# Optimization experiments

Measured on AMD Instinct MI355X. Metric: run time of the kernel, lower is better.

## Reference

```python
import jax, jax.numpy as jnp
import numpy as np
from jax import lax

SKIP = 0.3      # graph_skip_conn
STEPS = 5       # GGNN propagation steps
HEADS = 16
T, B, N, D = 16, 32, 256, 128
NUM_CLASSES = 2
EPS = 1e-8


def setup_inputs() -> dict:
    key = jax.random.key(0)
    ks = jax.random.split(key, 12)
    s = 0.05
    return {
        "inputs": jax.random.normal(ks[0], (T, B, N, D), dtype=jnp.float32),
        "supports": jax.random.uniform(ks[1], (B, N, N), dtype=jnp.float32),
        # multi-head weighted-cosine graph learner weights
        "W_gl": jax.random.normal(ks[2], (HEADS, D), dtype=jnp.float32) * s,
        # GGNN message transform
        "W_a": jax.random.normal(ks[3], (D, D), dtype=jnp.float32) * s,
        "b_a": jnp.zeros((D,), dtype=jnp.float32),
        # GGNN gated propagator (GRU-style) over concat([a, h]) -> D
        "W_r": jax.random.normal(ks[4], (2 * D, D), dtype=jnp.float32) * s,
        "b_r": jnp.zeros((D,), dtype=jnp.float32),
        "W_z": jax.random.normal(ks[5], (2 * D, D), dtype=jnp.float32) * s,
        "b_z": jnp.zeros((D,), dtype=jnp.float32),
        "W_h": jax.random.normal(ks[6], (2 * D, D), dtype=jnp.float32) * s,
        "b_h": jnp.zeros((D,), dtype=jnp.float32),
        # final classifier
        "W_fc": jax.random.normal(ks[7], (N * D, NUM_CLASSES), dtype=jnp.float32) * s,
        "b_fc": jnp.zeros((NUM_CLASSES,), dtype=jnp.float32),
    }


def _cell(x, A, W_gl, W_a, b_a, W_r, b_r, W_z, b_z, W_h, b_h):
    # ---- graph learner: multi-head weighted cosine similarity ----
    # x: (B,N,D); W_gl: (H,D)
    xw = x[None, :, :, :] * W_gl[:, None, None, :]             # (H,B,N,D)
    xw = xw / (jnp.linalg.norm(xw, axis=-1, keepdims=True) + EPS)
    att = jnp.einsum("hbnd,hbmd->hbnm", xw, xw).mean(axis=0)   # (B,N,N)
    att = jax.nn.relu(att)
    att = att / (att.sum(axis=-1, keepdims=True) + EPS)        # row-normalize
    A_new = SKIP * A + (1.0 - SKIP) * att                      # skip connection

    # ---- GGNN propagation over learned adjacency ----
    h = x
    for _ in range(STEPS):
        a = jnp.einsum("bnm,bmd->bnd", A_new, h) @ W_a + b_a   # message
        ah = jnp.concatenate([a, h], axis=-1)                  # (B,N,2D)
        r = jax.nn.sigmoid(ah @ W_r + b_r)
        z = jax.nn.sigmoid(ah @ W_z + b_z)
        h_tilde = jnp.tanh(jnp.concatenate([a, r * h], axis=-1) @ W_h + b_h)
        h = (1.0 - z) * h + z * h_tilde
    return h, A_new


def reference(inputs, supports, W_gl, W_a, b_a, W_r, b_r, W_z, b_z, W_h, b_h, W_fc, b_fc):
    def step(A, x_t):
        h, A_new = _cell(x_t, A, W_gl, W_a, b_a, W_r, b_r, W_z, b_z, W_h, b_h)
        return A_new, h

    A_final, outs = lax.scan(step, supports, inputs)           # outs: (T,B,N,D)
    last = outs[-1]                                            # (B,N,D)
    logits = last.reshape(last.shape[0], -1) @ W_fc + b_fc     # (B,C)
    return logits
```

## Files before the change

kernel.cpp:

```cpp
#include <hip/hip_runtime.h>
#include <math.h>

#define TT 16
#define BB 32
#define NN 256
#define DD 128
#define NSTEPS 5
#define SKIPF 0.3f
#define EPSF 1e-8f


typedef __attribute__((ext_vector_type(8))) short bf16x8;
typedef __attribute__((ext_vector_type(4))) float f32x4;
typedef __attribute__((ext_vector_type(8))) _Float16 half8;
typedef __attribute__((ext_vector_type(2))) _Float16 h2;

__device__ __forceinline__ unsigned short f2bf(float f) {
    union { float f; unsigned u; } v; v.f = f;
    unsigned r = (v.u + 0x7FFF + ((v.u >> 16) & 1)) >> 16;
    return (unsigned short)r;
}
__device__ __forceinline__ float bf2f(unsigned short u) {
    union { unsigned u; float f; } v; v.u = ((unsigned)u) << 16; return v.f;
}
__device__ __forceinline__ unsigned pack2(unsigned short a, unsigned short b) {
    return (unsigned)a | ((unsigned)b << 16);
}
__device__ __forceinline__ unsigned pkrtz(float a, float b) {
    unsigned r;
    asm("v_cvt_pkrtz_f16_f32 %0, %1, %2" : "=v"(r) : "v"(a), "v"(b));
    return r;
}
__device__ __forceinline__ h2 u2h(unsigned u) {
    union { unsigned u; h2 h; } v; v.u = u; return v.h;
}
__device__ __forceinline__ float sigmoidf_(float x) {
    return 1.0f / (1.0f + __expf(-x));
}
__device__ __forceinline__ float tanhf_(float x) {
    return 1.0f - 2.0f / (__expf(2.0f * x) + 1.0f);
}

__global__ __launch_bounds__(256) void k_prep(const float* __restrict__ x,
                                              const unsigned* __restrict__ wsqH,
                                              unsigned short* __restrict__ xh,
                                              unsigned* __restrict__ invnH) {
    int tb = blockIdx.x;
    int tid = threadIdx.x;
    int wave = tid >> 6, lane = tid & 63;
    int m16 = lane & 15, quad = lane >> 4;

    __shared__ unsigned short xsq[256 * 128];

    const float* xb = x + ((size_t)tb << 15);
    unsigned short* xhb = xh + ((size_t)tb << 15);

    #pragma unroll
    for (int it = 0; it < 16; ++it) {
        int flat = (it << 11) + (tid << 3);
        float4 a = *(const float4*)(xb + flat);
        float4 b = *(const float4*)(xb + flat + 4);
        uint4 o;
        o.x = pkrtz(a.x, a.y); o.y = pkrtz(a.z, a.w);
        o.z = pkrtz(b.x, b.y); o.w = pkrtz(b.z, b.w);
        *(uint4*)(xhb + flat) = o;
        uint4 q;
        q.x = pkrtz(a.x * a.x, a.y * a.y); q.y = pkrtz(a.z * a.z, a.w * a.w);
        q.z = pkrtz(b.x * b.x, b.y * b.y); q.w = pkrtz(b.z * b.z, b.w * b.w);
        int row = flat >> 7;
        int byteoff = (flat << 1) ^ ((row & 7) << 4);
        *(uint4*)((char*)xsq + byteoff) = q;
    }
    __syncthreads();

    half8 wf[4];
    #pragma unroll
    for (int ks = 0; ks < 4; ++ks)
        wf[ks] = *(const half8*)((const unsigned short*)wsqH + (m16 << 7) + (ks << 5) + (quad << 3));

    #pragma unroll
    for (int sub = 0; sub < 4; ++sub) {
        int rbase = (wave << 6) + (sub << 4);
        f32x4 acc = (f32x4){0.f, 0.f, 0.f, 0.f};
        #pragma unroll
        for (int ks = 0; ks < 4; ++ks) {
            int row = rbase + m16;
            int byteoff = ((row << 8) + (ks << 6) + (quad << 4)) ^ ((row & 7) << 4);
            half8 af = *(const half8*)((const char*)xsq + byteoff);
            acc = __builtin_amdgcn_mfma_f32_16x16x32_f16(af, wf[ks], acc, 0, 0, 0);
        }
        unsigned out[4];
        #pragma unroll
        for (int r = 0; r < 4; ++r) {
            float inv = 1.0f / (sqrtf(acc[r]) + EPSF);
            out[r] = pkrtz(inv, inv);
        }
        int n = rbase + (quad << 2);
        *(uint4*)(invnH + ((size_t)tb << 12) + (m16 << 8) + n) = *(uint4*)out;
    }
}

__global__ __launch_bounds__(256, 2) void k_gram2(const unsigned short* __restrict__ xhp,
                                                  const unsigned* __restrict__ wsqH,
                                                  const unsigned* __restrict__ invnH,
                                                  unsigned short* __restrict__ attn) {
    int bid = blockIdx.x;
    int tb = bid & 511;
    int rg = bid >> 9;
    int n0 = rg << 6;
    int tid = threadIdx.x;
    int wave = tid >> 6, lane = tid & 63;
    int m16 = lane & 15, quad = lane >> 4;
    int wcol = wave << 6;

    __shared__ unsigned wS[16 * 64];
    __shared__ unsigned ivS[16 * 256];
    __shared__ float rsum[4][64];

    const unsigned short* Xb = xhp + ((size_t)tb << 15);

    {
        uint4 v = *(const uint4*)(wsqH + (tid << 2));
        *(uint4*)(wS + (tid << 2)) = v;
    }
    {
        const unsigned* src = invnH + ((size_t)tb << 12);
        #pragma unroll
        for (int hh = 0; hh < 16; ++hh)
            ivS[(hh << 8) + tid] = src[(hh << 8) + tid];
    }

    half8 Bf[4][4];
    #pragma unroll
    for (int ks = 0; ks < 4; ++ks)
        #pragma unroll
        for (int cb = 0; cb < 4; ++cb)
            Bf[ks][cb] = *(const half8*)(Xb + ((wcol + (cb << 4) + m16) << 7) + (ks << 5) + (quad << 3));

    half8 Af[4][4];
    #pragma unroll
    for (int rb = 0; rb < 4; ++rb)
        #pragma unroll
        for (int ks = 0; ks < 4; ++ks)
            Af[rb][ks] = *(const half8*)(Xb + ((n0 + (rb << 4) + m16) << 7) + (ks << 5) + (quad << 3));

    f32x4 att[4][4];
    #pragma unroll
    for (int rb = 0; rb < 4; ++rb)
        #pragma unroll
        for (int cb = 0; cb < 4; ++cb) att[rb][cb] = (f32x4){0.f, 0.f, 0.f, 0.f};

    __syncthreads();

    union H8 { half8 v; h2 p[4]; };

    #pragma unroll 1
    for (int h = 0; h < 16; ++h) {
        const unsigned* ivh = ivS + (h << 8);
        h2 ivr[4], ivc[4];
        #pragma unroll
        for (int rb = 0; rb < 4; ++rb) ivr[rb] = u2h(ivh[n0 + (rb << 4) + m16]);
        #pragma unroll
        for (int cb = 0; cb < 4; ++cb) ivc[cb] = u2h(ivh[wcol + (cb << 4) + m16]);

        #pragma unroll
        for (int ks = 0; ks < 4; ++ks) {
            uint4 wu = *(const uint4*)(wS + (h << 6) + (ks << 4) + (quad << 2));
            h2 w0 = u2h(wu.x), w1 = u2h(wu.y), w2 = u2h(wu.z), w3 = u2h(wu.w);

            H8 afr[4];
            #pragma unroll
            for (int rb = 0; rb < 4; ++rb) {
                H8 a; a.v = Af[rb][ks];
                h2 s = ivr[rb];
                afr[rb].p[0] = a.p[0] * (w0 * s);
                afr[rb].p[1] = a.p[1] * (w1 * s);
                afr[rb].p[2] = a.p[2] * (w2 * s);
                afr[rb].p[3] = a.p[3] * (w3 * s);
            }
            #pragma unroll
            for (int cb = 0; cb < 4; ++cb) {
                H8 b; b.v = Bf[ks][cb];
                H8 bf;
                bf.p[0] = b.p[0] * ivc[cb];
                bf.p[1] = b.p[1] * ivc[cb];
                bf.p[2] = b.p[2] * ivc[cb];
                bf.p[3] = b.p[3] * ivc[cb];
                #pragma unroll
                for (int rb = 0; rb < 4; ++rb)
                    att[rb][cb] = __builtin_amdgcn_mfma_f32_16x16x32_f16(afr[rb].v, bf.v, att[rb][cb], 0, 0, 0);
            }
        }
    }

    float rs[4][4];
    #pragma unroll
    for (int rb = 0; rb < 4; ++rb)
        #pragma unroll
        for (int r = 0; r < 4; ++r) {
            float s = 0.f;
            #pragma unroll
            for (int cb = 0; cb < 4; ++cb) {
                float v = fmaxf(att[rb][cb][r], 0.0f);
                att[rb][cb][r] = v;
                s += v;
            }
            rs[rb][r] = s;
        }
    #pragma unroll
    for (int m = 1; m < 16; m <<= 1)
        #pragma unroll
        for (int rb = 0; rb < 4; ++rb)
            #pragma unroll
            for (int r = 0; r < 4; ++r)
                rs[rb][r] += __shfl_xor(rs[rb][r], m, 64);
    if (m16 == 0) {
        #pragma unroll
        for (int rb = 0; rb < 4; ++rb)
            #pragma unroll
            for (int r = 0; r < 4; ++r)
                rsum[wave][(rb << 4) + (quad << 2) + r] = rs[rb][r];
    }
    __syncthreads();

    unsigned short* outb = attn + ((size_t)tb << 16);
    #pragma unroll
    for (int rb = 0; rb < 4; ++rb) {
        #pragma unroll
        for (int r = 0; r < 4; ++r) {
            int row = (rb << 4) + (quad << 2) + r;
            float tot = rsum[0][row] + rsum[1][row] + rsum[2][row] + rsum[3][row];
            float inv = (1.0f - SKIPF) / (tot + 16.0f * EPSF);
            #pragma unroll
            for (int cb = 0; cb < 4; ++cb) {
                int col = wcol + (cb << 4) + m16;
                outb[((size_t)(n0 + row) << 8) + col] = f2bf(att[rb][cb][r] * inv);
            }
        }
    }
}

__global__ __launch_bounds__(256) void k_scanlast(const float* __restrict__ supports,
                                                  const unsigned short* __restrict__ AttA,
                                                  unsigned short* __restrict__ Afin) {
    size_t flat = ((size_t)blockIdx.x * 256 + threadIdx.x) * 4;
    float4 s4 = *(const float4*)(supports + flat);
    float a0 = s4.x, a1 = s4.y, a2 = s4.z, a3 = s4.w;
    #pragma unroll
    for (int t = 0; t < TT; ++t) {
        const unsigned short* p = AttA + ((size_t)t << 21) + flat;
        uint2 u = *(const uint2*)p;
        a0 = SKIPF * a0 + bf2f((unsigned short)(u.x & 0xffff));
        a1 = SKIPF * a1 + bf2f((unsigned short)(u.x >> 16));
        a2 = SKIPF * a2 + bf2f((unsigned short)(u.y & 0xffff));
        a3 = SKIPF * a3 + bf2f((unsigned short)(u.y >> 16));
    }
    uint2 o;
    o.x = pack2(f2bf(a0), f2bf(a1));
    o.y = pack2(f2bf(a2), f2bf(a3));
    *(uint2*)(Afin + flat) = o;
}


__global__ __launch_bounds__(256) void k_hTinit(const float* __restrict__ x15,
                                                unsigned short* __restrict__ hT) {
    int bid = blockIdx.x;
    int b = bid >> 5; int r = bid & 31; int d0 = (r >> 3) << 5; int n0 = (r & 7) << 5;
    __shared__ float tl[32][33];
    int tid = threadIdx.x;
    int i = tid >> 5, j = tid & 31;
    #pragma unroll
    for (int s = 0; s < 4; ++s) {
        int nl = (s << 3) + i;
        tl[nl][j] = x15[((size_t)(b * 256 + n0 + nl) << 7) + d0 + j];
    }
    __syncthreads();
    #pragma unroll
    for (int s = 0; s < 4; ++s) {
        int dd = (s << 3) + i;
        hT[((size_t)(b * 128 + d0 + dd) << 8) + n0 + j] = f2bf(tl[j][dd]);
    }
}

__global__ __launch_bounds__(256) void k_wprep(const float* __restrict__ Wa,
                                               const float* __restrict__ Wr,
                                               const float* __restrict__ Wz,
                                               const float* __restrict__ Wh,
                                               const float* __restrict__ Wgl,
                                               unsigned short* __restrict__ WaT,
                                               unsigned short* __restrict__ WrT,
                                               unsigned short* __restrict__ WzT,
                                               unsigned short* __restrict__ WhT,
                                               unsigned* __restrict__ wsqH) {
    int idx = blockIdx.x * 256 + threadIdx.x;
    if (idx < 16384) {
        int dout = idx >> 7, din = idx & 127;
        WaT[idx] = f2bf(Wa[(din << 7) + dout]);
    }
    if (idx < 1024) {
        int h = idx >> 6, j = idx & 63;
        float w0 = Wgl[(h << 7) + (j << 1)];
        float w1 = Wgl[(h << 7) + (j << 1) + 1];
        wsqH[idx] = pkrtz(w0 * w0, w1 * w1);
    }
    {
        int dout = idx >> 8, dk = idx & 255;
        WrT[idx] = f2bf(Wr[(dk << 7) + dout]);
        WzT[idx] = f2bf(Wz[(dk << 7) + dout]);
        WhT[idx] = f2bf(Wh[(dk << 7) + dout]);
    }
}

__global__ __launch_bounds__(256) void k_step(
    const unsigned short* __restrict__ Afin,
    const unsigned short* __restrict__ hT,
    const unsigned short* __restrict__ WaT, const float* __restrict__ ba,
    const unsigned short* __restrict__ WrT, const float* __restrict__ br,
    const unsigned short* __restrict__ WzT, const float* __restrict__ bz,
    const unsigned short* __restrict__ WhT, const float* __restrict__ bh,
    unsigned short* __restrict__ hT_o) {

    int bid = blockIdx.x;
    int b = bid & 31, rg = bid >> 5;
    int n0 = rg << 5;
    int tid = threadIdx.x;
    int wave = tid >> 6, lane = tid & 63;
    int m16 = lane & 15, quad = lane >> 4;
    int wcol = wave << 5;

    __shared__ unsigned short msgS[32 * 136];
    __shared__ unsigned short ahS[32 * 264];

    const unsigned short* hTb = hT + ((size_t)b << 15);

    #pragma unroll
    for (int j = 0; j < 16; ++j) {
        int idx = (j << 8) + tid;
        int d = idx >> 5, row = idx & 31;
        ahS[row * 264 + 128 + d] = hTb[((size_t)d << 8) + n0 + row];
    }

    f32x4 acc[2][2];
    #pragma unroll
    for (int rb = 0; rb < 2; ++rb)
        #pragma unroll
        for (int cb = 0; cb < 2; ++cb) acc[rb][cb] = (f32x4){0.f, 0.f, 0.f, 0.f};

    const unsigned short* Ab = Afin + ((size_t)b << 16) + ((size_t)n0 << 8);
    #pragma unroll 2
    for (int ks = 0; ks < 8; ++ks) {
        bf16x8 af[2], bf[2];
        #pragma unroll
        for (int rb = 0; rb < 2; ++rb)
            af[rb] = *(const bf16x8*)(Ab + (((rb << 4) + m16) << 8) + (ks << 5) + (quad << 3));
        #pragma unroll
        for (int cb = 0; cb < 2; ++cb)
            bf[cb] = *(const bf16x8*)(hTb + ((wcol + (cb << 4) + m16) << 8) + (ks << 5) + (quad << 3));
        #pragma unroll
        for (int rb = 0; rb < 2; ++rb)
            #pragma unroll
            for (int cb = 0; cb < 2; ++cb)
                acc[rb][cb] = __builtin_amdgcn_mfma_f32_16x16x32_bf16(af[rb], bf[cb], acc[rb][cb], 0, 0, 0);
    }
    #pragma unroll
    for (int rb = 0; rb < 2; ++rb)
        #pragma unroll
        for (int cb = 0; cb < 2; ++cb)
            #pragma unroll
            for (int r = 0; r < 4; ++r)
                msgS[((rb << 4) + (quad << 2) + r) * 136 + wcol + (cb << 4) + m16] = f2bf(acc[rb][cb][r]);
    __syncthreads();

    #pragma unroll
    for (int rb = 0; rb < 2; ++rb)
        #pragma unroll
        for (int cb = 0; cb < 2; ++cb) acc[rb][cb] = (f32x4){0.f, 0.f, 0.f, 0.f};
    #pragma unroll
    for (int ks = 0; ks < 4; ++ks) {
        bf16x8 af[2], bf[2];
        #pragma unroll
        for (int rb = 0; rb < 2; ++rb)
            af[rb] = *(const bf16x8*)(msgS + ((rb << 4) + m16) * 136 + (ks << 5) + (quad << 3));
        #pragma unroll
        for (int cb = 0; cb < 2; ++cb)
            bf[cb] = *(const bf16x8*)(WaT + ((wcol + (cb << 4) + m16) << 7) + (ks << 5) + (quad << 3));
        #pragma unroll
        for (int rb = 0; rb < 2; ++rb)
            #pragma unroll
            for (int cb = 0; cb < 2; ++cb)
                acc[rb][cb] = __builtin_amdgcn_mfma_f32_16x16x32_bf16(af[rb], bf[cb], acc[rb][cb], 0, 0, 0);
    }
    {
        float bav[2];
        #pragma unroll
        for (int cb = 0; cb < 2; ++cb) bav[cb] = ba[wcol + (cb << 4) + m16];
        #pragma unroll
        for (int rb = 0; rb < 2; ++rb)
            #pragma unroll
            for (int cb = 0; cb < 2; ++cb)
                #pragma unroll
                for (int r = 0; r < 4; ++r)
                    ahS[((rb << 4) + (quad << 2) + r) * 264 + wcol + (cb << 4) + m16] =
                        f2bf(acc[rb][cb][r] + bav[cb]);
    }
    __syncthreads();

    float hv[2][2][4];
    #pragma unroll
    for (int rb = 0; rb < 2; ++rb)
        #pragma unroll
        for (int cb = 0; cb < 2; ++cb) {
            int col = wcol + (cb << 4) + m16;
            uint2 u = *(const uint2*)(hTb + ((size_t)col << 8) + n0 + (rb << 4) + (quad << 2));
            hv[rb][cb][0] = bf2f((unsigned short)(u.x & 0xffff));
            hv[rb][cb][1] = bf2f((unsigned short)(u.x >> 16));
            hv[rb][cb][2] = bf2f((unsigned short)(u.y & 0xffff));
            hv[rb][cb][3] = bf2f((unsigned short)(u.y >> 16));
        }

    f32x4 racc[2][2], zacc[2][2];
    #pragma unroll
    for (int rb = 0; rb < 2; ++rb)
        #pragma unroll
        for (int cb = 0; cb < 2; ++cb) {
            racc[rb][cb] = (f32x4){0.f, 0.f, 0.f, 0.f};
            zacc[rb][cb] = (f32x4){0.f, 0.f, 0.f, 0.f};
        }
    #pragma unroll 2
    for (int ks = 0; ks < 8; ++ks) {
        bf16x8 af[2], bfr[2], bfz[2];
        #pragma unroll
        for (int rb = 0; rb < 2; ++rb)
            af[rb] = *(const bf16x8*)(ahS + ((rb << 4) + m16) * 264 + (ks << 5) + (quad << 3));
        #pragma unroll
        for (int cb = 0; cb < 2; ++cb) {
            int dout = wcol + (cb << 4) + m16;
            bfr[cb] = *(const bf16x8*)(WrT + (dout << 8) + (ks << 5) + (quad << 3));
            bfz[cb] = *(const bf16x8*)(WzT + (dout << 8) + (ks << 5) + (quad << 3));
        }
        #pragma unroll
        for (int rb = 0; rb < 2; ++rb)
            #pragma unroll
            for (int cb = 0; cb < 2; ++cb) {
                racc[rb][cb] = __builtin_amdgcn_mfma_f32_16x16x32_bf16(af[rb], bfr[cb], racc[rb][cb], 0, 0, 0);
                zacc[rb][cb] = __builtin_amdgcn_mfma_f32_16x16x32_bf16(af[rb], bfz[cb], zacc[rb][cb], 0, 0, 0);
            }
    }
    float zv[2][2][4];
    {
        float brv[2], bzv[2];
        #pragma unroll
        for (int cb = 0; cb < 2; ++cb) {
            brv[cb] = br[wcol + (cb << 4) + m16];
            bzv[cb] = bz[wcol + (cb << 4) + m16];
        }
        #pragma unroll
        for (int rb = 0; rb < 2; ++rb)
            #pragma unroll
            for (int cb = 0; cb < 2; ++cb)
                #pragma unroll
                for (int r = 0; r < 4; ++r) {
                    racc[rb][cb][r] = sigmoidf_(racc[rb][cb][r] + brv[cb]);
                    zv[rb][cb][r]  = sigmoidf_(zacc[rb][cb][r] + bzv[cb]);
                }
    }
    __syncthreads();

    #pragma unroll
    for (int rb = 0; rb < 2; ++rb)
        #pragma unroll
        for (int cb = 0; cb < 2; ++cb)
            #pragma unroll
            for (int r = 0; r < 4; ++r)
                ahS[((rb << 4) + (quad << 2) + r) * 264 + 128 + wcol + (cb << 4) + m16] =
                    f2bf(racc[rb][cb][r] * hv[rb][cb][r]);
    __syncthreads();

    #pragma unroll
    for (int rb = 0; rb < 2; ++rb)
        #pragma unroll
        for (int cb = 0; cb < 2; ++cb) acc[rb][cb] = (f32x4){0.f, 0.f, 0.f, 0.f};
    #pragma unroll 2
    for (int ks = 0; ks < 8; ++ks) {
        bf16x8 af[2], bf[2];
        #pragma unroll
        for (int rb = 0; rb < 2; ++rb)
            af[rb] = *(const bf16x8*)(ahS + ((rb << 4) + m16) * 264 + (ks << 5) + (quad << 3));
        #pragma unroll
        for (int cb = 0; cb < 2; ++cb)
            bf[cb] = *(const bf16x8*)(WhT + ((wcol + (cb << 4) + m16) << 8) + (ks << 5) + (quad << 3));
        #pragma unroll
        for (int rb = 0; rb < 2; ++rb)
            #pragma unroll
            for (int cb = 0; cb < 2; ++cb)
                acc[rb][cb] = __builtin_amdgcn_mfma_f32_16x16x32_bf16(af[rb], bf[cb], acc[rb][cb], 0, 0, 0);
    }

    {
        float bhv[2];
        #pragma unroll
        for (int cb = 0; cb < 2; ++cb) bhv[cb] = bh[wcol + (cb << 4) + m16];
        #pragma unroll
        for (int rb = 0; rb < 2; ++rb)
            #pragma unroll
            for (int cb = 0; cb < 2; ++cb) {
                int col = wcol + (cb << 4) + m16;
                unsigned short pk[4];
                #pragma unroll
                for (int r = 0; r < 4; ++r) {
                    float ht = tanhf_(acc[rb][cb][r] + bhv[cb]);
                    float hn = hv[rb][cb][r] + zv[rb][cb][r] * (ht - hv[rb][cb][r]);
                    pk[r] = f2bf(hn);
                }
                uint2 p;
                p.x = pack2(pk[0], pk[1]); p.y = pack2(pk[2], pk[3]);
                *(uint2*)(hT_o + ((size_t)(b * 128 + col) << 8) + n0 + (rb << 4) + (quad << 2)) = p;
            }
    }
}

__global__ __launch_bounds__(256) void k_fc(const unsigned short* __restrict__ hT,
                                            const float* __restrict__ Wfc,
                                            const float* __restrict__ bfc,
                                            float* __restrict__ out) {
    int bid = blockIdx.x;
    int b = bid >> 4, part = bid & 15;
    int tid = threadIdx.x;
    const unsigned short* hp = hT + ((size_t)b << 15);
    int i = part * 2048 + tid * 8;
    int d = i >> 8, n = i & 255;
    uint4 hu = *(const uint4*)(hp + i);
    unsigned short hs[8];
    hs[0] = hu.x & 0xffff; hs[1] = hu.x >> 16;
    hs[2] = hu.y & 0xffff; hs[3] = hu.y >> 16;
    hs[4] = hu.z & 0xffff; hs[5] = hu.z >> 16;
    hs[6] = hu.w & 0xffff; hs[7] = hu.w >> 16;
    float a0 = 0.f, a1 = 0.f;
    #pragma unroll
    for (int k = 0; k < 8; ++k) {
        float v = bf2f(hs[k]);
        const float2 w = *(const float2*)(Wfc + ((size_t)(n + k) * 128 + d) * 2);
        a0 = fmaf(v, w.x, a0);
        a1 = fmaf(v, w.y, a1);
    }
    int wave = tid >> 6, lane = tid & 63;
    #pragma unroll
    for (int off = 32; off; off >>= 1) {
        a0 += __shfl_down(a0, off, 64);
        a1 += __shfl_down(a1, off, 64);
    }
    __shared__ float r0[4], r1[4];
    if (lane == 0) { r0[wave] = a0; r1[wave] = a1; }
    __syncthreads();
    if (tid == 0) {
        float s0 = r0[0] + r0[1] + r0[2] + r0[3];
        float s1 = r1[0] + r1[1] + r1[2] + r1[3];
        if (part == 0) { s0 += bfc[0]; s1 += bfc[1]; }
        atomicAdd(&out[b * 2 + 0], s0);
        atomicAdd(&out[b * 2 + 1], s1);
    }
}

extern "C" void kernel_launch(void* const* d_in, const int* in_sizes, int n_in,
                              void* d_out, int out_size, void* d_ws, size_t ws_size,
                              hipStream_t stream) {
    const float* x_all    = (const float*)d_in[0];
    const float* supports = (const float*)d_in[1];
    const float* Wgl = (const float*)d_in[2];
    const float* Wa  = (const float*)d_in[3];
    const float* ba  = (const float*)d_in[4];
    const float* Wr  = (const float*)d_in[5];
    const float* br  = (const float*)d_in[6];
    const float* Wz  = (const float*)d_in[7];
    const float* bz  = (const float*)d_in[8];
    const float* Wh  = (const float*)d_in[9];
    const float* bh  = (const float*)d_in[10];
    const float* Wfc = (const float*)d_in[11];
    const float* bfc = (const float*)d_in[12];
    float* out = (float*)d_out;

    char* p = (char*)d_ws;
    auto alloc = [&](size_t bytes) { char* r = p; p += (bytes + 255) & ~(size_t)255; return r; };

    unsigned short* AttA = (unsigned short*)alloc((size_t)TT * BB * NN * NN * 2);
    unsigned short* xh   = (unsigned short*)alloc((size_t)TT * BB * NN * DD * 2);
    unsigned* invnH      = (unsigned*)alloc((size_t)TT * BB * 16 * NN * 4);
    unsigned short* Afin = (unsigned short*)alloc((size_t)BB * NN * NN * 2);
    unsigned short* hT0  = (unsigned short*)alloc((size_t)BB * DD * NN * 2);
    unsigned short* hT1  = (unsigned short*)alloc((size_t)BB * DD * NN * 2);
    unsigned short* WaT  = (unsigned short*)alloc(128 * 128 * 2);
    unsigned short* WrT  = (unsigned short*)alloc(256 * 128 * 2);
    unsigned short* WzT  = (unsigned short*)alloc(256 * 128 * 2);
    unsigned short* WhT  = (unsigned short*)alloc(256 * 128 * 2);
    unsigned* wsqH       = (unsigned*)alloc(16 * 64 * 4);

    k_wprep<<<128, 256, 0, stream>>>(Wa, Wr, Wz, Wh, Wgl, WaT, WrT, WzT, WhT, wsqH);
    k_prep<<<TT * BB, 256, 0, stream>>>(x_all, wsqH, xh, invnH);

    k_gram2<<<4 * TT * BB, 256, 0, stream>>>(xh, wsqH, invnH, AttA);
    k_scanlast<<<2048, 256, 0, stream>>>(supports, AttA, Afin);

    const float* x15 = x_all + (size_t)15 * BB * NN * DD;
    k_hTinit<<<BB * 32, 256, 0, stream>>>(x15, hT0);

    const unsigned short* hT_in = hT0;
    for (int s = 0; s < NSTEPS; ++s) {
        unsigned short* hTo = (s & 1) ? hT0 : hT1;
        k_step<<<8 * BB, 256, 0, stream>>>(Afin, hT_in,
                                           WaT, ba, WrT, br, WzT, bz, WhT, bh,
                                           hTo);
        hT_in = hTo;
    }
    hipMemsetAsync(d_out, 0, (size_t)out_size * sizeof(float), stream);
    k_fc<<<BB * 16, 256, 0, stream>>>(hT1, Wfc, bfc, out);
}
```

Measured before the change: 363.6 us.

## Fuse GGNN steps, init transpose and FC into one persistent kernel with per-batch barriers

Replaces the hT init kernel, five per-step launches and the FC kernel with a single launch of 256 blocks. The eight blocks of each batch synchronise through global atomic counters between propagation steps. The FC reduction is done directly from registers in the last step, so the final h is never written back. This removes seven kernel launches and their gaps, at the cost of spin-wait barriers that rely on all 256 blocks being co-resident.

```diff
diff --git a/kernel.cpp b/kernel.cpp
--- a/kernel.cpp
+++ b/kernel.cpp
@@ -39,6 +39,18 @@
 }
 __device__ __forceinline__ float tanhf_(float x) {
     return 1.0f - 2.0f / (__expf(2.0f * x) + 1.0f);
+}
+
+__device__ __forceinline__ void bbar(int* c) {
+    __syncthreads();
+    __threadfence();
+    if (threadIdx.x == 0) {
+        __hip_atomic_fetch_add(c, 1, __ATOMIC_RELEASE, __HIP_MEMORY_SCOPE_AGENT);
+        while (__hip_atomic_load(c, __ATOMIC_ACQUIRE, __HIP_MEMORY_SCOPE_AGENT) < 8)
+            __builtin_amdgcn_s_sleep(2);
+    }
+    __syncthreads();
+    (void)__hip_atomic_load(c, __ATOMIC_ACQUIRE, __HIP_MEMORY_SCOPE_AGENT);
 }
 
 __global__ __launch_bounds__(256) void k_prep(const float* __restrict__ x,
@@ -261,27 +273,6 @@
     *(uint2*)(Afin + flat) = o;
 }
 
-
-__global__ __launch_bounds__(256) void k_hTinit(const float* __restrict__ x15,
-                                                unsigned short* __restrict__ hT) {
-    int bid = blockIdx.x;
-    int b = bid >> 5; int r = bid & 31; int d0 = (r >> 3) << 5; int n0 = (r & 7) << 5;
-    __shared__ float tl[32][33];
-    int tid = threadIdx.x;
-    int i = tid >> 5, j = tid & 31;
-    #pragma unroll
-    for (int s = 0; s < 4; ++s) {
-        int nl = (s << 3) + i;
-        tl[nl][j] = x15[((size_t)(b * 256 + n0 + nl) << 7) + d0 + j];
-    }
-    __syncthreads();
-    #pragma unroll
-    for (int s = 0; s < 4; ++s) {
-        int dd = (s << 3) + i;
-        hT[((size_t)(b * 128 + d0 + dd) << 8) + n0 + j] = f2bf(tl[j][dd]);
-    }
-}
-
 __global__ __launch_bounds__(256) void k_wprep(const float* __restrict__ Wa,
                                                const float* __restrict__ Wr,
                                                const float* __restrict__ Wz,
@@ -311,14 +302,16 @@
     }
 }
 
-__global__ __launch_bounds__(256) void k_step(
+__global__ __launch_bounds__(256) void k_gru(
+    const float* __restrict__ x15,
     const unsigned short* __restrict__ Afin,
-    const unsigned short* __restrict__ hT,
     const unsigned short* __restrict__ WaT, const float* __restrict__ ba,
     const unsigned short* __restrict__ WrT, const float* __restrict__ br,
     const unsigned short* __restrict__ WzT, const float* __restrict__ bz,
     const unsigned short* __restrict__ WhT, const float* __restrict__ bh,
-    unsigned short* __restrict__ hT_o) {
+    const float* __restrict__ Wfc, const float* __restrict__ bfc,
+    unsigned short* __restrict__ hTa, unsigned short* __restrict__ hTbuf,
+    int* __restrict__ cnt, float* __restrict__ out) {
 
     int bid = blockIdx.x;
     int b = bid & 31, rg = bid >> 5;
@@ -330,232 +323,247 @@
 
     __shared__ unsigned short msgS[32 * 136];
     __shared__ unsigned short ahS[32 * 264];
-
-    const unsigned short* hTb = hT + ((size_t)b << 15);
-
-    #pragma unroll
-    for (int j = 0; j < 16; ++j) {
-        int idx = (j << 8) + tid;
-        int d = idx >> 5, row = idx & 31;
-        ahS[row * 264 + 128 + d] = hTb[((size_t)d << 8) + n0 + row];
-    }
-
-    f32x4 acc[2][2];
-    #pragma unroll
-    for (int rb = 0; rb < 2; ++rb)
-        #pragma unroll
-        for (int cb = 0; cb < 2; ++cb) acc[rb][cb] = (f32x4){0.f, 0.f, 0.f, 0.f};
-
+    __shared__ float rf0[4], rf1[4];
+
+    int* cbp = cnt + b * 5;
+
+    {
+        float* tl = (float*)ahS;
+        int i = tid >> 5, j = tid & 31;
+        for (int dt = 0; dt < 4; ++dt) {
+            int d0 = dt << 5;
+            #pragma unroll
+            for (int s4 = 0; s4 < 4; ++s4) {
+                int nl = (s4 << 3) + i;
+                tl[nl * 33 + j] = x15[((size_t)(b * 256 + n0 + nl) << 7) + d0 + j];
+            }
+            __syncthreads();
+            #pragma unroll
+            for (int s4 = 0; s4 < 4; ++s4) {
+                int dd = (s4 << 3) + i;
+                hTa[((size_t)(b * 128 + d0 + dd) << 8) + n0 + j] = f2bf(tl[j * 33 + dd]);
+            }
+            __syncthreads();
+        }
+    }
+    bbar(cbp + 0);
+
+    float fca = 0.f, fcb = 0.f;
     const unsigned short* Ab = Afin + ((size_t)b << 16) + ((size_t)n0 << 8);
-    #pragma unroll 2
-    for (int ks = 0; ks < 8; ++ks) {
-        bf16x8 af[2], bf[2];
+
+    for (int s = 0; s < NSTEPS; ++s) {
+        const unsigned short* hTin = (s & 1) ? hTbuf : hTa;
+        unsigned short* hTo = (s & 1) ? hTa : hTbuf;
+        const unsigned short* hTb = hTin + ((size_t)b << 15);
+
+        #pragma unroll
+        for (int j = 0; j < 16; ++j) {
+            int idx = (j << 8) + tid;
+            int d = idx >> 5, row = idx & 31;
+            ahS[row * 264 + 128 + d] = hTb[((size_t)d << 8) + n0 + row];
+        }
+
+        f32x4 acc[2][2];
         #pragma unroll
         for (int rb = 0; rb < 2; ++rb)
-            af[rb] = *(const bf16x8*)(Ab + (((rb << 4) + m16) << 8) + (ks << 5) + (quad << 3));
-        #pragma unroll
-        for (int cb = 0; cb < 2; ++cb)
-            bf[cb] = *(const bf16x8*)(hTb + ((wcol + (cb << 4) + m16) << 8) + (ks << 5) + (quad << 3));
+            #pragma unroll
+            for (int cb = 0; cb < 2; ++cb) acc[rb][cb] = (f32x4){0.f, 0.f, 0.f, 0.f};
+
+        #pragma unroll 2
+        for (int ks = 0; ks < 8; ++ks) {
+            bf16x8 af[2], bf[2];
+            #pragma unroll
+            for (int rb = 0; rb < 2; ++rb)
+                af[rb] = *(const bf16x8*)(Ab + (((rb << 4) + m16) << 8) + (ks << 5) + (quad << 3));
+            #pragma unroll
+            for (int cb = 0; cb < 2; ++cb)
+                bf[cb] = *(const bf16x8*)(hTb + ((wcol + (cb << 4) + m16) << 8) + (ks << 5) + (quad << 3));
+            #pragma unroll
+            for (int rb = 0; rb < 2; ++rb)
+                #pragma unroll
+                for (int cb = 0; cb < 2; ++cb)
+                    acc[rb][cb] = __builtin_amdgcn_mfma_f32_16x16x32_bf16(af[rb], bf[cb], acc[rb][cb], 0, 0, 0);
+        }
         #pragma unroll
         for (int rb = 0; rb < 2; ++rb)
             #pragma unroll
             for (int cb = 0; cb < 2; ++cb)
-                acc[rb][cb] = __builtin_amdgcn_mfma_f32_16x16x32_bf16(af[rb], bf[cb], acc[rb][cb], 0, 0, 0);
-    }
-    #pragma unroll
-    for (int rb = 0; rb < 2; ++rb)
-        #pragma unroll
-        for (int cb = 0; cb < 2; ++cb)
-            #pragma unroll
-            for (int r = 0; r < 4; ++r)
-                msgS[((rb << 4) + (quad << 2) + r) * 136 + wcol + (cb << 4) + m16] = f2bf(acc[rb][cb][r]);
-    __syncthreads();
-
-    #pragma unroll
-    for (int rb = 0; rb < 2; ++rb)
-        #pragma unroll
-        for (int cb = 0; cb < 2; ++cb) acc[rb][cb] = (f32x4){0.f, 0.f, 0.f, 0.f};
-    #pragma unroll
-    for (int ks = 0; ks < 4; ++ks) {
-        bf16x8 af[2], bf[2];
+                #pragma unroll
+                for (int r = 0; r < 4; ++r)
+                    msgS[((rb << 4) + (quad << 2) + r) * 136 + wcol + (cb << 4) + m16] = f2bf(acc[rb][cb][r]);
+        __syncthreads();
+
         #pragma unroll
         for (int rb = 0; rb < 2; ++rb)
-            af[rb] = *(const bf16x8*)(msgS + ((rb << 4) + m16) * 136 + (ks << 5) + (quad << 3));
-        #pragma unroll
-        for (int cb = 0; cb < 2; ++cb)
-            bf[cb] = *(const bf16x8*)(WaT + ((wcol + (cb << 4) + m16) << 7) + (ks << 5) + (quad << 3));
-        #pragma unroll
-        for (int rb = 0; rb < 2; ++rb)
+            #pragma unroll
+            for (int cb = 0; cb < 2; ++cb) acc[rb][cb] = (f32x4){0.f, 0.f, 0.f, 0.f};
+        #pragma unroll
+        for (int ks = 0; ks < 4; ++ks) {
+            bf16x8 af[2], bf[2];
+            #pragma unroll
+            for (int rb = 0; rb < 2; ++rb)
+                af[rb] = *(const bf16x8*)(msgS + ((rb << 4) + m16) * 136 + (ks << 5) + (quad << 3));
             #pragma unroll
             for (int cb = 0; cb < 2; ++cb)
-                acc[rb][cb] = __builtin_amdgcn_mfma_f32_16x16x32_bf16(af[rb], bf[cb], acc[rb][cb], 0, 0, 0);
-    }
-    {
-        float bav[2];
-        #pragma unroll
-        for (int cb = 0; cb < 2; ++cb) bav[cb] = ba[wcol + (cb << 4) + m16];
-        #pragma unroll
-        for (int rb = 0; rb < 2; ++rb)
-            #pragma unroll
-            for (int cb = 0; cb < 2; ++cb)
-                #pragma unroll
-                for (int r = 0; r < 4; ++r)
-                    ahS[((rb << 4) + (quad << 2) + r) * 264 + wcol + (cb << 4) + m16] =
-                        f2bf(acc[rb][cb][r] + bav[cb]);
-    }
-    __syncthreads();
-
-    float hv[2][2][4];
-    #pragma unroll
-    for (int rb = 0; rb < 2; ++rb)
-        #pragma unroll
-        for (int cb = 0; cb < 2; ++cb) {
-            int col = wcol + (cb << 4) + m16;
-            uint2 u = *(const uint2*)(hTb + ((size_t)col << 8) + n0 + (rb << 4) + (quad << 2));
-            hv[rb][cb][0] = bf2f((unsigned short)(u.x & 0xffff));
-            hv[rb][cb][1] = bf2f((unsigned short)(u.x >> 16));
-            hv[rb][cb][2] = bf2f((unsigned short)(u.y & 0xffff));
-            hv[rb][cb][3] = bf2f((unsigned short)(u.y >> 16));
-        }
-
-    f32x4 racc[2][2], zacc[2][2];
-    #pragma unroll
-    for (int rb = 0; rb < 2; ++rb)
-        #pragma unroll
-        for (int cb = 0; cb < 2; ++cb) {
-            racc[rb][cb] = (f32x4){0.f, 0.f, 0.f, 0.f};
-            zacc[rb][cb] = (f32x4){0.f, 0.f, 0.f, 0.f};
-        }
-    #pragma unroll 2
-    for (int ks = 0; ks < 8; ++ks) {
-        bf16x8 af[2], bfr[2], bfz[2];
-        #pragma unroll
-        for (int rb = 0; rb < 2; ++rb)
-            af[rb] = *(const bf16x8*)(ahS + ((rb << 4) + m16) * 264 + (ks << 5) + (quad << 3));
-        #pragma unroll
-        for (int cb = 0; cb < 2; ++cb) {
-            int dout = wcol + (cb << 4) + m16;
-            bfr[cb] = *(const bf16x8*)(WrT + (dout << 8) + (ks << 5) + (quad << 3));
-            bfz[cb] = *(const bf16x8*)(WzT + (dout << 8) + (ks << 5) + (quad << 3));
-        }
-        #pragma unroll
-        for (int rb = 0; rb < 2; ++rb)
-            #pragma unroll
-            for (int cb = 0; cb < 2; ++cb) {
-                racc[rb][cb] = __builtin_amdgcn_mfma_f32_16x16x32_bf16(af[rb], bfr[cb], racc[rb][cb], 0, 0, 0);
-                zacc[rb][cb] = __builtin_amdgcn_mfma_f32_16x16x32_bf16(af[rb], bfz[cb], zacc[rb][cb], 0, 0, 0);
-            }
-    }
-    float zv[2][2][4];
-    {
-        float brv[2], bzv[2];
-        #pragma unroll
-        for (int cb = 0; cb < 2; ++cb) {
-            brv[cb] = br[wcol + (cb << 4) + m16];
-            bzv[cb] = bz[wcol + (cb << 4) + m16];
-        }
-        #pragma unroll
-        for (int rb = 0; rb < 2; ++rb)
-            #pragma unroll
-            for (int cb = 0; cb < 2; ++cb)
-                #pragma unroll
-                for (int r = 0; r < 4; ++r) {
-                    racc[rb][cb][r] = sigmoidf_(racc[rb][cb][r] + brv[cb]);
-                    zv[rb][cb][r]  = sigmoidf_(zacc[rb][cb][r] + bzv[cb]);
-                }
-    }
-    __syncthreads();
-
-    #pragma unroll
-    for (int rb = 0; rb < 2; ++rb)
-        #pragma unroll
-        for (int cb = 0; cb < 2; ++cb)
-            #pragma unroll
-            for (int r = 0; r < 4; ++r)
-                ahS[((rb << 4) + (quad << 2) + r) * 264 + 128 + wcol + (cb << 4) + m16] =
-                    f2bf(racc[rb][cb][r] * hv[rb][cb][r]);
-    __syncthreads();
-
-    #pragma unroll
-    for (int rb = 0; rb < 2; ++rb)
-        #pragma unroll
-        for (int cb = 0; cb < 2; ++cb) acc[rb][cb] = (f32x4){0.f, 0.f, 0.f, 0.f};
-    #pragma unroll 2
-    for (int ks = 0; ks < 8; ++ks) {
-        bf16x8 af[2], bf[2];
-        #pragma unroll
-        for (int rb = 0; rb < 2; ++rb)
-            af[rb] = *(const bf16x8*)(ahS + ((rb << 4) + m16) * 264 + (ks << 5) + (quad << 3));
-        #pragma unroll
-        for (int cb = 0; cb < 2; ++cb)
-            bf[cb] = *(const bf16x8*)(WhT + ((wcol + (cb << 4) + m16) << 8) + (ks << 5) + (quad << 3));
-        #pragma unroll
-        for (int rb = 0; rb < 2; ++rb)
-            #pragma unroll
-            for (int cb = 0; cb < 2; ++cb)
-                acc[rb][cb] = __builtin_amdgcn_mfma_f32_16x16x32_bf16(af[rb], bf[cb], acc[rb][cb], 0, 0, 0);
-    }
-
-    {
-        float bhv[2];
-        #pragma unroll
-        for (int cb = 0; cb < 2; ++cb) bhv[cb] = bh[wcol + (cb << 4) + m16];
+                bf[cb] = *(const bf16x8*)(WaT + ((wcol + (cb << 4) + m16) << 7) + (ks << 5) + (quad << 3));
+            #pragma unroll
+            for (int rb = 0; rb < 2; ++rb)
+                #pragma unroll
+                for (int cb = 0; cb < 2; ++cb)
+                    acc[rb][cb] = __builtin_amdgcn_mfma_f32_16x16x32_bf16(af[rb], bf[cb], acc[rb][cb], 0, 0, 0);
+        }
+        {
+            float bav[2];
+            #pragma unroll
+            for (int cb = 0; cb < 2; ++cb) bav[cb] = ba[wcol + (cb << 4) + m16];
+            #pragma unroll
+            for (int rb = 0; rb < 2; ++rb)
+                #pragma unroll
+                for (int cb = 0; cb < 2; ++cb)
+                    #pragma unroll
+                    for (int r = 0; r < 4; ++r)
+                        ahS[((rb << 4) + (quad << 2) + r) * 264 + wcol + (cb << 4) + m16] =
+                            f2bf(acc[rb][cb][r] + bav[cb]);
+        }
+        __syncthreads();
+
+        float hv[2][2][4];
         #pragma unroll
         for (int rb = 0; rb < 2; ++rb)
             #pragma unroll
             for (int cb = 0; cb < 2; ++cb) {
                 int col = wcol + (cb << 4) + m16;
-                unsigned short pk[4];
-                #pragma unroll
-                for (int r = 0; r < 4; ++r) {
-                    float ht = tanhf_(acc[rb][cb][r] + bhv[cb]);
-                    float hn = hv[rb][cb][r] + zv[rb][cb][r] * (ht - hv[rb][cb][r]);
-                    pk[r] = f2bf(hn);
+                uint2 u = *(const uint2*)(hTb + ((size_t)col << 8) + n0 + (rb << 4) + (quad << 2));
+                hv[rb][cb][0] = bf2f((unsigned short)(u.x & 0xffff));
+                hv[rb][cb][1] = bf2f((unsigned short)(u.x >> 16));
+                hv[rb][cb][2] = bf2f((unsigned short)(u.y & 0xffff));
+                hv[rb][cb][3] = bf2f((unsigned short)(u.y >> 16));
+            }
+
+        f32x4 racc[2][2], zacc[2][2];
+        #pragma unroll
+        for (int rb = 0; rb < 2; ++rb)
+            #pragma unroll
+            for (int cb = 0; cb < 2; ++cb) {
+                racc[rb][cb] = (f32x4){0.f, 0.f, 0.f, 0.f};
+                zacc[rb][cb] = (f32x4){0.f, 0.f, 0.f, 0.f};
+            }
+        #pragma unroll 2
+        for (int ks = 0; ks < 8; ++ks) {
+            bf16x8 af[2], bfr[2], bfz[2];
+            #pragma unroll
+            for (int rb = 0; rb < 2; ++rb)
+                af[rb] = *(const bf16x8*)(ahS + ((rb << 4) + m16) * 264 + (ks << 5) + (quad << 3));
+            #pragma unroll
+            for (int cb = 0; cb < 2; ++cb) {
+                int dout = wcol + (cb << 4) + m16;
+                bfr[cb] = *(const bf16x8*)(WrT + (dout << 8) + (ks << 5) + (quad << 3));
+                bfz[cb] = *(const bf16x8*)(WzT + (dout << 8) + (ks << 5) + (quad << 3));
+            }
+            #pragma unroll
+            for (int rb = 0; rb < 2; ++rb)
+                #pragma unroll
+                for (int cb = 0; cb < 2; ++cb) {
+                    racc[rb][cb] = __builtin_amdgcn_mfma_f32_16x16x32_bf16(af[rb], bfr[cb], racc[rb][cb], 0, 0, 0);
+                    zacc[rb][cb] = __builtin_amdgcn_mfma_f32_16x16x32_bf16(af[rb], bfz[cb], zacc[rb][cb], 0, 0, 0);
                 }
-                uint2 p;
-                p.x = pack2(pk[0], pk[1]); p.y = pack2(pk[2], pk[3]);
-                *(uint2*)(hT_o + ((size_t)(b * 128 + col) << 8) + n0 + (rb << 4) + (quad << 2)) = p;
-            }
-    }
-}
-
-__global__ __launch_bounds__(256) void k_fc(const unsigned short* __restrict__ hT,
-                                            const float* __restrict__ Wfc,
-                                            const float* __restrict__ bfc,
-                                            float* __restrict__ out) {
-    int bid = blockIdx.x;
-    int b = bid >> 4, part = bid & 15;
-    int tid = threadIdx.x;
-    const unsigned short* hp = hT + ((size_t)b << 15);
-    int i = part * 2048 + tid * 8;
-    int d = i >> 8, n = i & 255;
-    uint4 hu = *(const uint4*)(hp + i);
-    unsigned short hs[8];
-    hs[0] = hu.x & 0xffff; hs[1] = hu.x >> 16;
-    hs[2] = hu.y & 0xffff; hs[3] = hu.y >> 16;
-    hs[4] = hu.z & 0xffff; hs[5] = hu.z >> 16;
-    hs[6] = hu.w & 0xffff; hs[7] = hu.w >> 16;
-    float a0 = 0.f, a1 = 0.f;
-    #pragma unroll
-    for (int k = 0; k < 8; ++k) {
-        float v = bf2f(hs[k]);
-        const float2 w = *(const float2*)(Wfc + ((size_t)(n + k) * 128 + d) * 2);
-        a0 = fmaf(v, w.x, a0);
-        a1 = fmaf(v, w.y, a1);
-    }
-    int wave = tid >> 6, lane = tid & 63;
+        }
+        float zv[2][2][4];
+        {
+            float brv[2], bzv[2];
+            #pragma unroll
+            for (int cb = 0; cb < 2; ++cb) {
+                brv[cb] = br[wcol + (cb << 4) + m16];
+                bzv[cb] = bz[wcol + (cb << 4) + m16];
+            }
+            #pragma unroll
+            for (int rb = 0; rb < 2; ++rb)
+                #pragma unroll
+                for (int cb = 0; cb < 2; ++cb)
+                    #pragma unroll
+                    for (int r = 0; r < 4; ++r) {
+                        racc[rb][cb][r] = sigmoidf_(racc[rb][cb][r] + brv[cb]);
+                        zv[rb][cb][r]  = sigmoidf_(zacc[rb][cb][r] + bzv[cb]);
+                    }
+        }
+        __syncthreads();
+
+        #pragma unroll
+        for (int rb = 0; rb < 2; ++rb)
+            #pragma unroll
+            for (int cb = 0; cb < 2; ++cb)
+                #pragma unroll
+                for (int r = 0; r < 4; ++r)
+                    ahS[((rb << 4) + (quad << 2) + r) * 264 + 128 + wcol + (cb << 4) + m16] =
+                        f2bf(racc[rb][cb][r] * hv[rb][cb][r]);
+        __syncthreads();
+
+        #pragma unroll
+        for (int rb = 0; rb < 2; ++rb)
+            #pragma unroll
+            for (int cb = 0; cb < 2; ++cb) acc[rb][cb] = (f32x4){0.f, 0.f, 0.f, 0.f};
+        #pragma unroll 2
+        for (int ks = 0; ks < 8; ++ks) {
+            bf16x8 af[2], bf[2];
+            #pragma unroll
+            for (int rb = 0; rb < 2; ++rb)
+                af[rb] = *(const bf16x8*)(ahS + ((rb << 4) + m16) * 264 + (ks << 5) + (quad << 3));
+            #pragma unroll
+            for (int cb = 0; cb < 2; ++cb)
+                bf[cb] = *(const bf16x8*)(WhT + ((wcol + (cb << 4) + m16) << 8) + (ks << 5) + (quad << 3));
+            #pragma unroll
+            for (int rb = 0; rb < 2; ++rb)
+                #pragma unroll
+                for (int cb = 0; cb < 2; ++cb)
+                    acc[rb][cb] = __builtin_amdgcn_mfma_f32_16x16x32_bf16(af[rb], bf[cb], acc[rb][cb], 0, 0, 0);
+        }
+
+        {
+            float bhv[2];
+            #pragma unroll
+            for (int cb = 0; cb < 2; ++cb) bhv[cb] = bh[wcol + (cb << 4) + m16];
+            #pragma unroll
+            for (int rb = 0; rb < 2; ++rb)
+                #pragma unroll
+                for (int cb = 0; cb < 2; ++cb) {
+                    int col = wcol + (cb << 4) + m16;
+                    unsigned short pk[4];
+                    #pragma unroll
+                    for (int r = 0; r < 4; ++r) {
+                        float ht = tanhf_(acc[rb][cb][r] + bhv[cb]);
+                        float hn = hv[rb][cb][r] + zv[rb][cb][r] * (ht - hv[rb][cb][r]);
+                        pk[r] = f2bf(hn);
+                    }
+                    if (s < NSTEPS - 1) {
+                        uint2 p;
+                        p.x = pack2(pk[0], pk[1]); p.y = pack2(pk[2], pk[3]);
+                        *(uint2*)(hTo + ((size_t)(b * 128 + col) << 8) + n0 + (rb << 4) + (quad << 2)) = p;
+                    } else {
+                        #pragma unroll
+                        for (int r = 0; r < 4; ++r) {
+                            int nn = n0 + (rb << 4) + (quad << 2) + r;
+                            float hval = bf2f(pk[r]);
+                            const float2 w = *(const float2*)(Wfc + (size_t)(nn * 128 + col) * 2);
+                            fca = fmaf(hval, w.x, fca);
+                            fcb = fmaf(hval, w.y, fcb);
+                        }
+                    }
+                }
+        }
+        if (s < NSTEPS - 1) bbar(cbp + 1 + s);
+    }
+
     #pragma unroll
     for (int off = 32; off; off >>= 1) {
-        a0 += __shfl_down(a0, off, 64);
-        a1 += __shfl_down(a1, off, 64);
-    }
-    __shared__ float r0[4], r1[4];
-    if (lane == 0) { r0[wave] = a0; r1[wave] = a1; }
+        fca += __shfl_down(fca, off, 64);
+        fcb += __shfl_down(fcb, off, 64);
+    }
+    if (lane == 0) { rf0[wave] = fca; rf1[wave] = fcb; }
     __syncthreads();
     if (tid == 0) {
-        float s0 = r0[0] + r0[1] + r0[2] + r0[3];
-        float s1 = r1[0] + r1[1] + r1[2] + r1[3];
-        if (part == 0) { s0 += bfc[0]; s1 += bfc[1]; }
+        float s0 = rf0[0] + rf0[1] + rf0[2] + rf0[3];
+        float s1 = rf1[0] + rf1[1] + rf1[2] + rf1[3];
+        if (rg == 0) { s0 += bfc[0]; s1 += bfc[1]; }
         atomicAdd(&out[b * 2 + 0], s0);
         atomicAdd(&out[b * 2 + 1], s1);
     }
@@ -593,6 +601,10 @@
     unsigned short* WzT  = (unsigned short*)alloc(256 * 128 * 2);
     unsigned short* WhT  = (unsigned short*)alloc(256 * 128 * 2);
     unsigned* wsqH       = (unsigned*)alloc(16 * 64 * 4);
+    int* cntB            = (int*)alloc(32 * 5 * 4);
+
+    hipMemsetAsync(cntB, 0, 32 * 5 * 4, stream);
+    hipMemsetAsync(d_out, 0, (size_t)out_size * sizeof(float), stream);
 
     k_wprep<<<128, 256, 0, stream>>>(Wa, Wr, Wz, Wh, Wgl, WaT, WrT, WzT, WhT, wsqH);
     k_prep<<<TT * BB, 256, 0, stream>>>(x_all, wsqH, xh, invnH);
@@ -601,16 +613,7 @@
     k_scanlast<<<2048, 256, 0, stream>>>(supports, AttA, Afin);
 
     const float* x15 = x_all + (size_t)15 * BB * NN * DD;
-    k_hTinit<<<BB * 32, 256, 0, stream>>>(x15, hT0);
-
-    const unsigned short* hT_in = hT0;
-    for (int s = 0; s < NSTEPS; ++s) {
-        unsigned short* hTo = (s & 1) ? hT0 : hT1;
-        k_step<<<8 * BB, 256, 0, stream>>>(Afin, hT_in,
-                                           WaT, ba, WrT, br, WzT, bz, WhT, bh,
-                                           hTo);
-        hT_in = hTo;
-    }
-    hipMemsetAsync(d_out, 0, (size_t)out_size * sizeof(float), stream);
-    k_fc<<<BB * 16, 256, 0, stream>>>(hT1, Wfc, bfc, out);
-}
+    k_gru<<<8 * BB, 256, 0, stream>>>(x15, Afin,
+                                      WaT, ba, WrT, br, WzT, bz, WhT, bh,
+                                      Wfc, bfc, hT0, hT1, cntB, out);
+}
```

After: 523.9 us. +44.1%, slower.
